# Kernel optimization log

Hardware: AMD Instinct MI355X
Metric: run time of the kernel (lower is better)

## Reference

```python
import jax, jax.numpy as jnp
import numpy as np

N_NODES = 50000
N_EDGES = 800000
DIMS = [128, 128, 128, 64]  # in, hid1, hid2, out
EPS = 1e-12


def setup_inputs() -> dict:
    key = jax.random.key(0)
    ks = jax.random.split(key, 32)
    inp = {
        "x": jax.random.normal(ks[0], (N_NODES, DIMS[0]), dtype=jnp.float32),
        "edge_src": jax.random.randint(ks[1], (N_EDGES,), 0, N_NODES),
        "edge_dst": jax.random.randint(ks[2], (N_EDGES,), 0, N_NODES),
    }
    k = 3
    for l in range(3):
        din, dout = DIMS[l], DIMS[l + 1]
        s_in = 1.0 / np.sqrt(din)
        inp[f"Wp{l+1}"] = jax.random.uniform(ks[k], (din, din), jnp.float32, -s_in, s_in); k += 1
        inp[f"bp{l+1}"] = jax.random.uniform(ks[k], (din,), jnp.float32, -s_in, s_in); k += 1
        inp[f"Ws{l+1}"] = jax.random.uniform(ks[k], (din, dout), jnp.float32, -s_in, s_in); k += 1
        inp[f"Wn{l+1}"] = jax.random.uniform(ks[k], (din, dout), jnp.float32, -s_in, s_in); k += 1
        inp[f"b{l+1}"] = jnp.zeros((dout,), jnp.float32); k += 1
    return inp


def _sage_pool_layer(x, src, dst, Wp, bp, Ws, Wn, b):
    # per-edge: relu(fc_pool(x_src)); [E, din]
    m = jax.nn.relu(x[src] @ Wp + bp)
    # max-pool over in-neighbors of each dst node; [N, din]
    pooled = jax.ops.segment_max(m, dst, num_segments=x.shape[0])
    deg = jax.ops.segment_sum(jnp.ones((dst.shape[0],), x.dtype), dst,
                              num_segments=x.shape[0])
    pooled = jnp.where(deg[:, None] > 0, pooled, 0.0)  # zero-degree -> 0 (DGL)
    return x @ Ws + pooled @ Wn + b


def _l2norm_relu(h):
    n = jnp.sqrt(jnp.sum(h * h, axis=1, keepdims=True))
    return jax.nn.relu(h / jnp.maximum(n, EPS))


def reference(x, edge_src, edge_dst,
              Wp1, bp1, Ws1, Wn1, b1,
              Wp2, bp2, Ws2, Wn2, b2,
              Wp3, bp3, Ws3, Wn3, b3):
    h = _l2norm_relu(_sage_pool_layer(x, edge_src, edge_dst, Wp1, bp1, Ws1, Wn1, b1))
    h = _l2norm_relu(_sage_pool_layer(h, edge_src, edge_dst, Wp2, bp2, Ws2, Wn2, b2))
    h = _l2norm_relu(_sage_pool_layer(h, edge_src, edge_dst, Wp3, bp3, Ws3, Wn3, b3))
    return h
```

## Files before the change

### kernel.cpp

```cpp
#include <hip/hip_runtime.h>
#include <math.h>

#define N_NODES 50000
#define N_EDGES 800000
#define CAP 64
#define RANGES 8
#define NODES_PER_RANGE 6250
#define CSRB 1024
#define GEMMB 782
#define LROW 136

typedef __attribute__((ext_vector_type(8))) short short8;
typedef __attribute__((ext_vector_type(2))) short short2v;
typedef __attribute__((ext_vector_type(4))) float f32x4;

__device__ __forceinline__ unsigned short f2bf(float f) {
    unsigned int u = __float_as_uint(f);
    return (unsigned short)((u + 0x7FFFu + ((u >> 16) & 1u)) >> 16);
}

template <bool F32>
__device__ __forceinline__ short8 loadA(const void* A, int off) {
    short8 r;
    if (F32) {
        const float* p = (const float*)A + off;
        float4 f0 = *(const float4*)p;
        float4 f1 = *(const float4*)(p + 4);
        r[0] = (short)f2bf(f0.x); r[1] = (short)f2bf(f0.y);
        r[2] = (short)f2bf(f0.z); r[3] = (short)f2bf(f0.w);
        r[4] = (short)f2bf(f1.x); r[5] = (short)f2bf(f1.y);
        r[6] = (short)f2bf(f1.z); r[7] = (short)f2bf(f1.w);
    } else {
        r = *(const short8*)((const unsigned short*)A + off);
    }
    return r;
}

struct WDescs { const float* W[9]; int N[9]; };

__global__ __launch_bounds__(256) void prep_kernel(
    WDescs wd, unsigned short* __restrict__ Wpk, int* __restrict__ deg)
{
    const int nthr = gridDim.x * 256;
    const int tid = blockIdx.x * 256 + threadIdx.x;
    for (int id = tid; id < 9 * 16384; id += nthr) {
        int mi = id >> 14;
        int loc = id & 16383;
        int N = wd.N[mi];
        if (loc < 128 * N) {
            int c = loc / (N * 32);
            int n = (loc - c * N * 32) >> 5;
            int k = c * 32 + (loc & 31);
            Wpk[mi * 16384 + loc] = f2bf(wd.W[mi][k * N + n]);
        }
    }
    for (int i = tid; i < N_NODES; i += nthr) deg[i] = 0;
}

__global__ __launch_bounds__(256) void mix_kernel(
    const int* __restrict__ esrc, const int* __restrict__ edst,
    int* __restrict__ deg, unsigned short* __restrict__ csr16,
    const float* __restrict__ x, const unsigned short* __restrict__ Wp1,
    const float* __restrict__ bp1, unsigned short* __restrict__ Y)
{
    if (blockIdx.x < CSRB) {
        int range = blockIdx.x & (RANGES - 1);
        for (int cb = blockIdx.x >> 3; cb < N_EDGES / 256; cb += CSRB / 8) {
            int e = cb * 256 + threadIdx.x;
            int d = edst[e];
            if ((unsigned)(d - range * NODES_PER_RANGE) < (unsigned)NODES_PER_RANGE) {
                int r = atomicAdd(&deg[d], 1);
                if (r < CAP) csr16[(d << 6) + r] = (unsigned short)esrc[e];
            }
        }
        return;
    }
    const int tile = blockIdx.x - CSRB;
    const int lane = threadIdx.x & 63;
    const int wv = threadIdx.x >> 6;
    const int cl = lane & 15;
    const int quad = lane >> 4;
    const int rowBase = tile * 64 + wv * 16;
    const int ar = min(rowBase + cl, N_NODES - 1);
    const int bLane = cl * 32 + quad * 8;

    f32x4 acc[8];
    #pragma unroll
    for (int t = 0; t < 8; ++t) acc[t] = (f32x4){0.f, 0.f, 0.f, 0.f};

    #pragma unroll
    for (int c = 0; c < 4; ++c) {
        short8 af = loadA<true>(x, ar * 128 + c * 32 + quad * 8);
        const unsigned short* Bc = Wp1 + c * 4096 + bLane;
        #pragma unroll
        for (int t = 0; t < 8; ++t) {
            short8 bf = *(const short8*)(Bc + t * 512);
            acc[t] = __builtin_amdgcn_mfma_f32_16x16x32_bf16(af, bf, acc[t], 0, 0, 0);
        }
    }
    const int row0 = rowBase + quad * 4;
    #pragma unroll
    for (int t = 0; t < 8; ++t) {
        float bc = bp1[t * 16 + cl];
        #pragma unroll
        for (int g = 0; g < 4; ++g) {
            int r = row0 + g;
            if (r < N_NODES)
                Y[r * 128 + t * 16 + cl] = f2bf(fmaxf(acc[t][g] + bc, 0.0f));
        }
    }
}

__global__ __launch_bounds__(256) void pool_max8(
    const unsigned short* __restrict__ y, const int* __restrict__ deg,
    const unsigned short* __restrict__ csr16, unsigned short* __restrict__ pool)
{
    const int wv = threadIdx.x >> 6;
    const int d = threadIdx.x & 63;
    const int n = blockIdx.x * 4 + wv;
    const int e0 = n << 6;
    const int e1 = e0 + min(deg[n], CAP);
    const unsigned short* yb = y + 2 * d;

    short2v acc = (short2v){0, 0};
    int e = e0;
    for (; e + 8 <= e1; e += 8) {
        int s0 = csr16[e + 0], s1 = csr16[e + 1];
        int s2 = csr16[e + 2], s3 = csr16[e + 3];
        int s4 = csr16[e + 4], s5 = csr16[e + 5];
        int s6 = csr16[e + 6], s7 = csr16[e + 7];
        short2v v0 = *(const short2v*)(yb + (s0 << 7));
        short2v v1 = *(const short2v*)(yb + (s1 << 7));
        short2v v2 = *(const short2v*)(yb + (s2 << 7));
        short2v v3 = *(const short2v*)(yb + (s3 << 7));
        short2v v4 = *(const short2v*)(yb + (s4 << 7));
        short2v v5 = *(const short2v*)(yb + (s5 << 7));
        short2v v6 = *(const short2v*)(yb + (s6 << 7));
        short2v v7 = *(const short2v*)(yb + (s7 << 7));
        acc = __builtin_elementwise_max(acc, v0);
        acc = __builtin_elementwise_max(acc, v1);
        acc = __builtin_elementwise_max(acc, v2);
        acc = __builtin_elementwise_max(acc, v3);
        acc = __builtin_elementwise_max(acc, v4);
        acc = __builtin_elementwise_max(acc, v5);
        acc = __builtin_elementwise_max(acc, v6);
        acc = __builtin_elementwise_max(acc, v7);
    }
    for (; e < e1; ++e) {
        int s = csr16[e];
        short2v v = *(const short2v*)(yb + (s << 7));
        acc = __builtin_elementwise_max(acc, v);
    }
    *(short2v*)(pool + n * 128 + 2 * d) = acc;
}

template <bool A0F32, bool LAST>
__global__ __launch_bounds__(256) void dualy_kernel(
    const void* __restrict__ A0,
    const unsigned short* __restrict__ B0, const unsigned short* __restrict__ B1,
    const float* __restrict__ bias,
    const unsigned short* __restrict__ PL,
    unsigned short* __restrict__ outH, float* __restrict__ outF,
    const unsigned short* __restrict__ Bnext, const float* __restrict__ bnext,
    unsigned short* __restrict__ Yout)
{
    constexpr int NT = LAST ? 4 : 8;
    constexpr int N = NT * 16;
    __shared__ unsigned short lds[4][16 * LROW];

    const int lane = threadIdx.x & 63;
    const int wv = threadIdx.x >> 6;
    const int cl = lane & 15;
    const int quad = lane >> 4;
    const int nodeBase = blockIdx.x * 64 + wv * 16;
    unsigned short* plw = &lds[wv][0];

    const int ar = min(nodeBase + cl, N_NODES - 1);
    const int aBase = ar * 128 + quad * 8;
    const int bLane = cl * 32 + quad * 8;

    f32x4 acc[NT];
    #pragma unroll
    for (int t = 0; t < NT; ++t) acc[t] = (f32x4){0.f, 0.f, 0.f, 0.f};

    #pragma unroll
    for (int c = 0; c < 4; ++c) {
        short8 a0 = loadA<A0F32>(A0, aBase + c * 32);
        short8 a1 = *(const short8*)(PL + aBase + c * 32);
        const unsigned short* B0c = B0 + c * (N * 32) + bLane;
        const unsigned short* B1c = B1 + c * (N * 32) + bLane;
        #pragma unroll
        for (int t = 0; t < NT; ++t) {
            short8 bf = *(const short8*)(B0c + t * 512);
            acc[t] = __builtin_amdgcn_mfma_f32_16x16x32_bf16(a0, bf, acc[t], 0, 0, 0);
        }
        #pragma unroll
        for (int t = 0; t < NT; ++t) {
            short8 bf = *(const short8*)(B1c + t * 512);
            acc[t] = __builtin_amdgcn_mfma_f32_16x16x32_bf16(a1, bf, acc[t], 0, 0, 0);
        }
    }

    #pragma unroll
    for (int t = 0; t < NT; ++t) {
        float bc = bias[t * 16 + cl];
        #pragma unroll
        for (int g = 0; g < 4; ++g) acc[t][g] += bc;
    }

    float inv[4];
    #pragma unroll
    for (int g = 0; g < 4; ++g) {
        float s = 0.f;
        #pragma unroll
        for (int t = 0; t < NT; ++t) s += acc[t][g] * acc[t][g];
        s += __shfl_xor(s, 1, 64);
        s += __shfl_xor(s, 2, 64);
        s += __shfl_xor(s, 4, 64);
        s += __shfl_xor(s, 8, 64);
        inv[g] = 1.0f / fmaxf(sqrtf(s), 1e-12f);
    }

    const int row0 = nodeBase + quad * 4;

    if (LAST) {
        #pragma unroll
        for (int t = 0; t < NT; ++t)
            #pragma unroll
            for (int g = 0; g < 4; ++g) {
                int r = row0 + g;
                if (r < N_NODES)
                    outF[r * N + t * 16 + cl] = fmaxf(acc[t][g] * inv[g], 0.0f);
            }
        return;
    }

    #pragma unroll
    for (int t = 0; t < NT; ++t)
        #pragma unroll
        for (int g = 0; g < 4; ++g) {
            int r = row0 + g;
            unsigned short h = f2bf(fmaxf(acc[t][g] * inv[g], 0.0f));
            if (r < N_NODES) outH[r * 128 + t * 16 + cl] = h;
            plw[(quad * 4 + g) * LROW + t * 16 + cl] = h;
        }

    f32x4 ya[8];
    #pragma unroll
    for (int t = 0; t < 8; ++t) ya[t] = (f32x4){0.f, 0.f, 0.f, 0.f};
    #pragma unroll
    for (int c = 0; c < 4; ++c) {
        short8 af = *(const short8*)(plw + cl * LROW + c * 32 + quad * 8);
        const unsigned short* Bc = Bnext + c * 4096 + bLane;
        #pragma unroll
        for (int t = 0; t < 8; ++t) {
            short8 bf = *(const short8*)(Bc + t * 512);
            ya[t] = __builtin_amdgcn_mfma_f32_16x16x32_bf16(af, bf, ya[t], 0, 0, 0);
        }
    }
    #pragma unroll
    for (int t = 0; t < 8; ++t) {
        float bc = bnext[t * 16 + cl];
        #pragma unroll
        for (int g = 0; g < 4; ++g) {
            int r = row0 + g;
            if (r < N_NODES)
                Yout[r * 128 + t * 16 + cl] = f2bf(fmaxf(ya[t][g] + bc, 0.0f));
        }
    }
}

extern "C" void kernel_launch(void* const* d_in, const int* in_sizes, int n_in,
                              void* d_out, int out_size, void* d_ws, size_t ws_size,
                              hipStream_t stream) {
    const float* x    = (const float*)d_in[0];
    const int*   esrc = (const int*)d_in[1];
    const int*   edst = (const int*)d_in[2];
    const float* Wp[3], *bp[3], *Ws[3], *Wn[3], *bb[3];
    for (int l = 0; l < 3; ++l) {
        Wp[l] = (const float*)d_in[3 + 5 * l];
        bp[l] = (const float*)d_in[4 + 5 * l];
        Ws[l] = (const float*)d_in[5 + 5 * l];
        Wn[l] = (const float*)d_in[6 + 5 * l];
        bb[l] = (const float*)d_in[7 + 5 * l];
    }

    const int NF = N_NODES * 128;
    unsigned short* YA  = (unsigned short*)d_ws;
    unsigned short* YB  = YA + NF;
    unsigned short* PL  = YB + NF;
    unsigned short* H1  = PL + NF;
    unsigned short* H2  = H1 + NF;
    unsigned short* Wpk = H2 + NF;
    int* deg = (int*)(Wpk + 9 * 16384);
    unsigned short* csr16 = (unsigned short*)(deg + N_NODES);

    auto WH = [&](int i) { return Wpk + i * 16384; };

    WDescs wd;
    wd.W[0] = Wp[0]; wd.N[0] = 128;
    wd.W[1] = Ws[0]; wd.N[1] = 128;
    wd.W[2] = Wn[0]; wd.N[2] = 128;
    wd.W[3] = Wp[1]; wd.N[3] = 128;
    wd.W[4] = Ws[1]; wd.N[4] = 128;
    wd.W[5] = Wn[1]; wd.N[5] = 128;
    wd.W[6] = Wp[2]; wd.N[6] = 128;
    wd.W[7] = Ws[2]; wd.N[7] = 64;
    wd.W[8] = Wn[2]; wd.N[8] = 64;

    const int poolBlocks = N_NODES / 4;

    prep_kernel<<<576, 256, 0, stream>>>(wd, Wpk, deg);
    mix_kernel<<<CSRB + GEMMB, 256, 0, stream>>>(esrc, edst, deg, csr16,
                                                 x, WH(0), bp[0], YA);
    pool_max8<<<poolBlocks, 256, 0, stream>>>(YA, deg, csr16, PL);
    dualy_kernel<true, false><<<GEMMB, 256, 0, stream>>>(
        x, WH(1), WH(2), bb[0], PL, H1, nullptr, WH(3), bp[1], YB);
    pool_max8<<<poolBlocks, 256, 0, stream>>>(YB, deg, csr16, PL);
    dualy_kernel<false, false><<<GEMMB, 256, 0, stream>>>(
        H1, WH(4), WH(5), bb[1], PL, H2, nullptr, WH(6), bp[2], YA);
    pool_max8<<<poolBlocks, 256, 0, stream>>>(YA, deg, csr16, PL);
    dualy_kernel<false, true><<<GEMMB, 256, 0, stream>>>(
        H2, WH(7), WH(8), bb[2], PL, nullptr, (float*)d_out,
        nullptr, nullptr, nullptr);
}
```

Measured before the change: 349.8 us.

## Split pool gather across wave halves with wider loads; flatten CSR build blocks

The max-pool kernel now splits each wave into two halves. Each half loads 4 bf16 values per lane and handles alternate groups of 4 neighbors, with indices read as packed uint2. The halves are then combined by a cross-half shuffle and max. The intent is to halve the number of gather instructions per edge and widen memory accesses. Separately, the CSR-building part of mix_kernel drops its grid-stride loop for one block per (edge chunk, range) pair and places the GEMM blocks first in the grid. This launches far more small blocks, adding launch and scheduling overhead.

```diff
diff --git a/kernel.cpp b/kernel.cpp
--- a/kernel.cpp
+++ b/kernel.cpp
@@ -6,12 +6,12 @@
 #define CAP 64
 #define RANGES 8
 #define NODES_PER_RANGE 6250
-#define CSRB 1024
 #define GEMMB 782
+#define CSRB (N_EDGES / 256 * RANGES)
 #define LROW 136
 
 typedef __attribute__((ext_vector_type(8))) short short8;
-typedef __attribute__((ext_vector_type(2))) short short2v;
+typedef __attribute__((ext_vector_type(4))) short short4v;
 typedef __attribute__((ext_vector_type(4))) float f32x4;
 
 __device__ __forceinline__ unsigned short f2bf(float f) {
@@ -63,19 +63,18 @@
     const float* __restrict__ x, const unsigned short* __restrict__ Wp1,
     const float* __restrict__ bp1, unsigned short* __restrict__ Y)
 {
-    if (blockIdx.x < CSRB) {
-        int range = blockIdx.x & (RANGES - 1);
-        for (int cb = blockIdx.x >> 3; cb < N_EDGES / 256; cb += CSRB / 8) {
-            int e = cb * 256 + threadIdx.x;
-            int d = edst[e];
-            if ((unsigned)(d - range * NODES_PER_RANGE) < (unsigned)NODES_PER_RANGE) {
-                int r = atomicAdd(&deg[d], 1);
-                if (r < CAP) csr16[(d << 6) + r] = (unsigned short)esrc[e];
-            }
+    if (blockIdx.x >= GEMMB) {
+        int b = blockIdx.x - GEMMB;
+        int range = b & (RANGES - 1);
+        int e = (b >> 3) * 256 + threadIdx.x;
+        int d = edst[e];
+        if ((unsigned)(d - range * NODES_PER_RANGE) < (unsigned)NODES_PER_RANGE) {
+            int r = atomicAdd(&deg[d], 1);
+            if (r < CAP) csr16[(d << 6) + r] = (unsigned short)esrc[e];
         }
         return;
     }
-    const int tile = blockIdx.x - CSRB;
+    const int tile = blockIdx.x;
     const int lane = threadIdx.x & 63;
     const int wv = threadIdx.x >> 6;
     const int cl = lane & 15;
@@ -111,47 +110,47 @@
     }
 }
 
-__global__ __launch_bounds__(256) void pool_max8(
+__global__ __launch_bounds__(256) void pool_max4(
     const unsigned short* __restrict__ y, const int* __restrict__ deg,
     const unsigned short* __restrict__ csr16, unsigned short* __restrict__ pool)
 {
     const int wv = threadIdx.x >> 6;
-    const int d = threadIdx.x & 63;
+    const int lane = threadIdx.x & 63;
+    const int half = lane >> 5;
+    const int q = lane & 31;
     const int n = blockIdx.x * 4 + wv;
     const int e0 = n << 6;
     const int e1 = e0 + min(deg[n], CAP);
-    const unsigned short* yb = y + 2 * d;
-
-    short2v acc = (short2v){0, 0};
+    const unsigned short* yb = y + 4 * q;
+
+    short4v acc = (short4v){0, 0, 0, 0};
     int e = e0;
     for (; e + 8 <= e1; e += 8) {
-        int s0 = csr16[e + 0], s1 = csr16[e + 1];
-        int s2 = csr16[e + 2], s3 = csr16[e + 3];
-        int s4 = csr16[e + 4], s5 = csr16[e + 5];
-        int s6 = csr16[e + 6], s7 = csr16[e + 7];
-        short2v v0 = *(const short2v*)(yb + (s0 << 7));
-        short2v v1 = *(const short2v*)(yb + (s1 << 7));
-        short2v v2 = *(const short2v*)(yb + (s2 << 7));
-        short2v v3 = *(const short2v*)(yb + (s3 << 7));
-        short2v v4 = *(const short2v*)(yb + (s4 << 7));
-        short2v v5 = *(const short2v*)(yb + (s5 << 7));
-        short2v v6 = *(const short2v*)(yb + (s6 << 7));
-        short2v v7 = *(const short2v*)(yb + (s7 << 7));
-        acc = __builtin_elementwise_max(acc, v0);
-        acc = __builtin_elementwise_max(acc, v1);
-        acc = __builtin_elementwise_max(acc, v2);
-        acc = __builtin_elementwise_max(acc, v3);
-        acc = __builtin_elementwise_max(acc, v4);
-        acc = __builtin_elementwise_max(acc, v5);
-        acc = __builtin_elementwise_max(acc, v6);
-        acc = __builtin_elementwise_max(acc, v7);
+        uint2 I = *(const uint2*)(csr16 + e + (half << 2));
+        int sa = (int)(I.x & 0xFFFF), sb = (int)(I.x >> 16);
+        int sc = (int)(I.y & 0xFFFF), sd = (int)(I.y >> 16);
+        short4v va = *(const short4v*)(yb + (sa << 7));
+        short4v vb = *(const short4v*)(yb + (sb << 7));
+        short4v vc = *(const short4v*)(yb + (sc << 7));
+        short4v vd = *(const short4v*)(yb + (sd << 7));
+        acc = __builtin_elementwise_max(acc, va);
+        acc = __builtin_elementwise_max(acc, vb);
+        acc = __builtin_elementwise_max(acc, vc);
+        acc = __builtin_elementwise_max(acc, vd);
     }
     for (; e < e1; ++e) {
         int s = csr16[e];
-        short2v v = *(const short2v*)(yb + (s << 7));
+        short4v v = *(const short4v*)(yb + (s << 7));
         acc = __builtin_elementwise_max(acc, v);
     }
-    *(short2v*)(pool + n * 128 + 2 * d) = acc;
+    int2 ai = *(int2*)&acc;
+    int2 bi;
+    bi.x = __shfl_xor(ai.x, 32, 64);
+    bi.y = __shfl_xor(ai.y, 32, 64);
+    short4v other = *(short4v*)&bi;
+    acc = __builtin_elementwise_max(acc, other);
+    if (half == 0)
+        *(short4v*)(pool + n * 128 + 4 * q) = acc;
 }
 
 template <bool A0F32, bool LAST>
@@ -311,15 +310,15 @@
     const int poolBlocks = N_NODES / 4;
 
     prep_kernel<<<576, 256, 0, stream>>>(wd, Wpk, deg);
-    mix_kernel<<<CSRB + GEMMB, 256, 0, stream>>>(esrc, edst, deg, csr16,
+    mix_kernel<<<GEMMB + CSRB, 256, 0, stream>>>(esrc, edst, deg, csr16,
                                                  x, WH(0), bp[0], YA);
-    pool_max8<<<poolBlocks, 256, 0, stream>>>(YA, deg, csr16, PL);
+    pool_max4<<<poolBlocks, 256, 0, stream>>>(YA, deg, csr16, PL);
     dualy_kernel<true, false><<<GEMMB, 256, 0, stream>>>(
         x, WH(1), WH(2), bb[0], PL, H1, nullptr, WH(3), bp[1], YB);
-    pool_max8<<<poolBlocks, 256, 0, stream>>>(YB, deg, csr16, PL);
+    pool_max4<<<poolBlocks, 256, 0, stream>>>(YB, deg, csr16, PL);
     dualy_kernel<false, false><<<GEMMB, 256, 0, stream>>>(
         H1, WH(4), WH(5), bb[1], PL, H2, nullptr, WH(6), bp[2], YA);
-    pool_max8<<<poolBlocks, 256, 0, stream>>>(YA, deg, csr16, PL);
+    pool_max4<<<poolBlocks, 256, 0, stream>>>(YA, deg, csr16, PL);
     dualy_kernel<false, true><<<GEMMB, 256, 0, stream>>>(
         H2, WH(7), WH(8), bb[2], PL, nullptr, (float*)d_out,
         nullptr, nullptr, nullptr);
```

New measurement: 348.9 us. No clear change (-0.3%).
